# Kernel tuning notes

Measured on AMD Instinct MI355X. Metric: run time of the kernel, lower is better.

## Reference

```python
import jax, jax.numpy as jnp
import numpy as np

N = 50000
V_FEATS = 128
FILTERS = 128
K = 20


def setup_inputs() -> dict:
    key = jax.random.key(0)
    ks = jax.random.split(key, 8)
    vertices = jax.random.normal(ks[0], (N, V_FEATS), dtype=jnp.float32)
    nh_indices = jax.random.randint(ks[1], (N, K), 0, N, dtype=jnp.int32)
    int_idx = jax.random.randint(ks[2], (N, K), 0, N, dtype=jnp.int32)
    mask = jax.random.uniform(ks[3], (N, K)) < 0.3
    int_indices = jnp.where(mask, jnp.int32(-1), int_idx)
    nh_edges = jax.random.normal(ks[4], (N, K), dtype=jnp.float32)
    int_edges = jax.random.normal(ks[5], (N, K), dtype=jnp.float32)
    # kaiming-uniform-ish init for params
    bound = float(np.sqrt(6.0 / V_FEATS))
    Wvc = jax.random.uniform(ks[6], (V_FEATS, FILTERS), minval=-bound, maxval=bound, dtype=jnp.float32)
    Wvn = jax.random.uniform(ks[7], (V_FEATS, FILTERS), minval=-bound, maxval=bound, dtype=jnp.float32)
    bv = jnp.zeros((FILTERS,), dtype=jnp.float32)
    return {"vertices": vertices, "nh_indices": nh_indices, "int_indices": int_indices,
            "nh_edges": nh_edges, "int_edges": int_edges, "Wvc": Wvc, "Wvn": Wvn, "bv": bv}


def reference(vertices, nh_indices, int_indices, nh_edges, int_edges, Wvc, Wvn, bv):
    # [N, 2K] concatenated neighbor + interface indices / edge weights
    indices = jnp.concatenate([nh_indices, int_indices], axis=1)
    edges = jnp.concatenate([nh_edges, int_edges], axis=1)[..., None]  # [N,2K,1]
    part = (indices != -1).astype(vertices.dtype)[..., None]           # [N,2K,1] validity mask
    Zc = vertices @ Wvc                                                # [N,F] center term
    v_Wvn = vertices @ Wvn                                             # [N,F]
    gathered = v_Wvn[indices]  # [N,2K,F]; -1 wraps to last row, zeroed by mask (same as torch)
    denom = jnp.sum(indices > -1, axis=1, keepdims=True).astype(vertices.dtype)  # [N,1]
    Zn = jnp.sum(gathered * part * edges, axis=1) / denom             # [N,F]
    z = jax.nn.relu(Zc + Zn + bv)
    return z
```

## Files before the change

kernel.cpp:

```cpp
#include <hip/hip_runtime.h>

#define NV 50000
#define F 128
#define K 20
#define KCAT 256
#define RPB 32

typedef __attribute__((ext_vector_type(8))) __bf16 bf16x8;
typedef __attribute__((ext_vector_type(4))) float f32x4;
typedef __attribute__((ext_vector_type(2))) float f32x2;

__device__ inline ushort f2bf(float x) {
    uint u = __float_as_uint(x);
    return (ushort)((u + 0x7fffu + ((u >> 16) & 1u)) >> 16);
}


__global__ __launch_bounds__(256) void prep_kernel(
    const f32x4* __restrict__ v4, ushort* __restrict__ vb,
    uchar* __restrict__ v8,
    const float* __restrict__ Wvc, const float* __restrict__ Wvn,
    ushort* __restrict__ wt)
{
    int bid = blockIdx.x;
    if (bid < NV * F / 4 / 256) {
        int t = bid * 256 + threadIdx.x;
        int e = t * 4;
        int row = e >> 7, f = e & 127;
        f32x4 x = __builtin_nontemporal_load(v4 + t);
        uint2 o;
        o.x = (uint)f2bf(x[0]) | ((uint)f2bf(x[1]) << 16);
        o.y = (uint)f2bf(x[2]) | ((uint)f2bf(x[3]) << 16);
        *reinterpret_cast<uint2*>(vb + (size_t)row * KCAT + f) = o;
        int p8 = __builtin_amdgcn_cvt_pk_fp8_f32(x[0], x[1], 0, false);
        p8     = __builtin_amdgcn_cvt_pk_fp8_f32(x[2], x[3], p8, true);
        *reinterpret_cast<uint*>(v8 + (size_t)row * F + f) = (uint)p8;
    } else {
        int t = (bid - NV * F / 4 / 256) * 256 + threadIdx.x;
        int c = t >> 8, k = t & 255;
        float w = (k < F) ? Wvc[k * F + c] : Wvn[(k - F) * F + c];
        wt[t] = f2bf(w);
    }
}

__global__ __launch_bounds__(256) void agg_fp8(
    const uchar* __restrict__ v8,
    const int* __restrict__ nh_idx, const int* __restrict__ int_idx,
    const float* __restrict__ nh_e, const float* __restrict__ int_e,
    ushort* __restrict__ vb)
{
    __shared__ int2 sJW[RPB][2 * K + 1];
    __shared__ int  sCnt[RPB];

    const int tid = threadIdx.x;
    const int r0  = blockIdx.x * RPB;

    if (tid < RPB) sCnt[tid] = K;
    for (int x = tid; x < RPB * K; x += 256) {
        int r = x / K, k = x - r * K;
        int row = r0 + r;
        int2 jw = make_int2(0, 0);
        if (row < NV) {
            long g = (long)row * K + k;
            jw = make_int2(nh_idx[g], __float_as_int(nh_e[g]));
        }
        sJW[r][k] = jw;
    }
    __syncthreads();
    for (int x = tid; x < RPB * K; x += 256) {
        int r = x / K, k = x - r * K;
        int row = r0 + r;
        int2 jw = make_int2(0, 0);
        bool valid = false;
        if (row < NV) {
            long g = (long)row * K + k;
            int   j = int_idx[g];
            float w = int_e[g];
            valid = (j >= 0);
            jw = make_int2(valid ? j : 0, valid ? __float_as_int(w) : 0);
        }
        sJW[r][K + k] = jw;
        if (valid) atomicAdd(&sCnt[r], 1);
    }
    __syncthreads();

    const int lane  = tid & 63;
    const int wave  = tid >> 6;
    const int chunk = lane & 7;
    const int rw    = (wave << 3) + (lane >> 3);
    const uchar* __restrict__ src = v8 + chunk * 16;

    float acc[16];
    #pragma unroll
    for (int i = 0; i < 16; ++i) acc[i] = 0.f;

    #pragma unroll 4
    for (int k = 0; k < 2 * K; ++k) {
        int2  jw = sJW[rw][k];
        float w  = __int_as_float(jw.y);
        uint4 p  = *reinterpret_cast<const uint4*>(src + (size_t)jw.x * F);
        f32x2 f0 = __builtin_amdgcn_cvt_pk_f32_fp8(p.x, false);
        f32x2 f1 = __builtin_amdgcn_cvt_pk_f32_fp8(p.x, true);
        f32x2 f2 = __builtin_amdgcn_cvt_pk_f32_fp8(p.y, false);
        f32x2 f3 = __builtin_amdgcn_cvt_pk_f32_fp8(p.y, true);
        f32x2 f4 = __builtin_amdgcn_cvt_pk_f32_fp8(p.z, false);
        f32x2 f5 = __builtin_amdgcn_cvt_pk_f32_fp8(p.z, true);
        f32x2 f6 = __builtin_amdgcn_cvt_pk_f32_fp8(p.w, false);
        f32x2 f7 = __builtin_amdgcn_cvt_pk_f32_fp8(p.w, true);
        acc[0]  = fmaf(w, f0[0], acc[0]);   acc[1]  = fmaf(w, f0[1], acc[1]);
        acc[2]  = fmaf(w, f1[0], acc[2]);   acc[3]  = fmaf(w, f1[1], acc[3]);
        acc[4]  = fmaf(w, f2[0], acc[4]);   acc[5]  = fmaf(w, f2[1], acc[5]);
        acc[6]  = fmaf(w, f3[0], acc[6]);   acc[7]  = fmaf(w, f3[1], acc[7]);
        acc[8]  = fmaf(w, f4[0], acc[8]);   acc[9]  = fmaf(w, f4[1], acc[9]);
        acc[10] = fmaf(w, f5[0], acc[10]);  acc[11] = fmaf(w, f5[1], acc[11]);
        acc[12] = fmaf(w, f6[0], acc[12]);  acc[13] = fmaf(w, f6[1], acc[13]);
        acc[14] = fmaf(w, f7[0], acc[14]);  acc[15] = fmaf(w, f7[1], acc[15]);
    }

    const int row = r0 + rw;
    if (row < NV) {
        float inv = 1.f / (float)sCnt[rw];
        uint4 o0, o1;
        o0.x = (uint)f2bf(acc[0]  * inv) | ((uint)f2bf(acc[1]  * inv) << 16);
        o0.y = (uint)f2bf(acc[2]  * inv) | ((uint)f2bf(acc[3]  * inv) << 16);
        o0.z = (uint)f2bf(acc[4]  * inv) | ((uint)f2bf(acc[5]  * inv) << 16);
        o0.w = (uint)f2bf(acc[6]  * inv) | ((uint)f2bf(acc[7]  * inv) << 16);
        o1.x = (uint)f2bf(acc[8]  * inv) | ((uint)f2bf(acc[9]  * inv) << 16);
        o1.y = (uint)f2bf(acc[10] * inv) | ((uint)f2bf(acc[11] * inv) << 16);
        o1.z = (uint)f2bf(acc[12] * inv) | ((uint)f2bf(acc[13] * inv) << 16);
        o1.w = (uint)f2bf(acc[14] * inv) | ((uint)f2bf(acc[15] * inv) << 16);
        uint4* dst = reinterpret_cast<uint4*>(vb + (size_t)row * KCAT + F + chunk * 16);
        dst[0] = o0;
        dst[1] = o1;
    }
}

__global__ __launch_bounds__(256) void gemm_fused(
    const ushort* __restrict__ vb,
    const ushort* __restrict__ wt,
    const float* __restrict__ bv,
    float* __restrict__ out)
{
    const int lane = threadIdx.x & 63;
    const int wave = threadIdx.x >> 6;
    const int r0   = blockIdx.x * 64 + wave * 16;

    int arow = r0 + (lane & 15);
    if (arow >= NV) arow = NV - 1;

    const bf16x8* abase = reinterpret_cast<const bf16x8*>(
        vb + (size_t)arow * KCAT + (lane >> 4) * 8);
    bf16x8 a[8];
    #pragma unroll
    for (int ks = 0; ks < 8; ++ks)
        a[ks] = __builtin_nontemporal_load(abase + ks * 4);

    const ushort* wbase = wt + (size_t)(lane & 15) * KCAT + (lane >> 4) * 8;
    const int col0  = lane & 15;
    const int rbase = r0 + (lane >> 4) * 4;

    #pragma unroll 1
    for (int ct = 0; ct < 8; ++ct) {
        const bf16x8* wb = reinterpret_cast<const bf16x8*>(
            wbase + (size_t)ct * 16 * KCAT);
        f32x4 acc = (f32x4){0.f, 0.f, 0.f, 0.f};
        #pragma unroll
        for (int ks = 0; ks < 8; ++ks) {
            bf16x8 b = wb[ks * 4];
            acc = __builtin_amdgcn_mfma_f32_16x16x32_bf16(a[ks], b, acc, 0, 0, 0);
        }
        int c = ct * 16 + col0;
        float bb = bv[c];
        #pragma unroll
        for (int reg = 0; reg < 4; ++reg) {
            int r = rbase + reg;
            if (r < NV) {
                float z = acc[reg] + bb;
                __builtin_nontemporal_store(fmaxf(z, 0.f), out + (size_t)r * F + c);
            }
        }
    }
}

extern "C" void kernel_launch(void* const* d_in, const int* in_sizes, int n_in,
                              void* d_out, int out_size, void* d_ws, size_t ws_size,
                              hipStream_t stream)
{
    const float* v       = (const float*)d_in[0];
    const int*   nh_idx  = (const int*)  d_in[1];
    const int*   int_idx = (const int*)  d_in[2];
    const float* nh_e    = (const float*)d_in[3];
    const float* int_e   = (const float*)d_in[4];
    const float* Wvc     = (const float*)d_in[5];
    const float* Wvn     = (const float*)d_in[6];
    const float* bv      = (const float*)d_in[7];
    float* out = (float*)d_out;

    ushort* vb = (ushort*)d_ws;
    ushort* wt = vb + (size_t)NV * KCAT;
    uchar*  v8 = (uchar*)(wt + (size_t)F * KCAT);

    prep_kernel<<<NV * F / 4 / 256 + F * KCAT / 256, 256, 0, stream>>>(
        (const f32x4*)v, vb, v8, Wvc, Wvn, wt);
    agg_fp8<<<(NV + RPB - 1) / RPB, 256, 0, stream>>>(v8, nh_idx, int_idx,
                                                      nh_e, int_e, vb);
    gemm_fused<<<(NV + 63) / 64, 256, 0, stream>>>(vb, wt, bv, out);
}
```

Before: 156.2 us.

## Fuse neighbor aggregation and GEMM into one kernel via LDS staging

Merges the fp8 gather-aggregate kernel and the bf16 MFMA GEMM into one kernel. The aggregated rows are kept in shared memory instead of being written to and re-read from a global bf16 buffer. The center-term A operand is now read as fp32 and converted to bf16 inside the kernel, so the prep kernel no longer writes a bf16 copy of the vertices. Each block handles 64 rows in two aggregation passes, which saves a launch and global traffic at the cost of more LDS per block and possibly lower occupancy.

```diff
diff --git a/kernel.cpp b/kernel.cpp
--- a/kernel.cpp
+++ b/kernel.cpp
@@ -4,7 +4,8 @@
 #define F 128
 #define K 20
 #define KCAT 256
-#define RPB 32
+#define RPB 64
+#define LDSW (F + 8)
 
 typedef __attribute__((ext_vector_type(8))) __bf16 bf16x8;
 typedef __attribute__((ext_vector_type(4))) float f32x4;
@@ -17,8 +18,7 @@
 
 
 __global__ __launch_bounds__(256) void prep_kernel(
-    const f32x4* __restrict__ v4, ushort* __restrict__ vb,
-    uchar* __restrict__ v8,
+    const f32x4* __restrict__ v4, uchar* __restrict__ v8,
     const float* __restrict__ Wvc, const float* __restrict__ Wvn,
     ushort* __restrict__ wt)
 {
@@ -28,10 +28,6 @@
         int e = t * 4;
         int row = e >> 7, f = e & 127;
         f32x4 x = __builtin_nontemporal_load(v4 + t);
-        uint2 o;
-        o.x = (uint)f2bf(x[0]) | ((uint)f2bf(x[1]) << 16);
-        o.y = (uint)f2bf(x[2]) | ((uint)f2bf(x[3]) << 16);
-        *reinterpret_cast<uint2*>(vb + (size_t)row * KCAT + f) = o;
         int p8 = __builtin_amdgcn_cvt_pk_fp8_f32(x[0], x[1], 0, false);
         p8     = __builtin_amdgcn_cvt_pk_fp8_f32(x[2], x[3], p8, true);
         *reinterpret_cast<uint*>(v8 + (size_t)row * F + f) = (uint)p8;
@@ -43,14 +39,18 @@
     }
 }
 
-__global__ __launch_bounds__(256) void agg_fp8(
+__global__ __launch_bounds__(256) void fused_kernel(
+    const float* __restrict__ v,
     const uchar* __restrict__ v8,
     const int* __restrict__ nh_idx, const int* __restrict__ int_idx,
     const float* __restrict__ nh_e, const float* __restrict__ int_e,
-    ushort* __restrict__ vb)
+    const ushort* __restrict__ wt,
+    const float* __restrict__ bv,
+    float* __restrict__ out)
 {
-    __shared__ int2 sJW[RPB][2 * K + 1];
-    __shared__ int  sCnt[RPB];
+    __shared__ int2   sJW[RPB][2 * K + 1];
+    __shared__ int    sCnt[RPB];
+    __shared__ ushort sVA[RPB][LDSW];
 
     const int tid = threadIdx.x;
     const int r0  = blockIdx.x * RPB;
@@ -87,38 +87,37 @@
     const int lane  = tid & 63;
     const int wave  = tid >> 6;
     const int chunk = lane & 7;
-    const int rw    = (wave << 3) + (lane >> 3);
-    const uchar* __restrict__ src = v8 + chunk * 16;
-
-    float acc[16];
-    #pragma unroll
-    for (int i = 0; i < 16; ++i) acc[i] = 0.f;
-
-    #pragma unroll 4
-    for (int k = 0; k < 2 * K; ++k) {
-        int2  jw = sJW[rw][k];
-        float w  = __int_as_float(jw.y);
-        uint4 p  = *reinterpret_cast<const uint4*>(src + (size_t)jw.x * F);
-        f32x2 f0 = __builtin_amdgcn_cvt_pk_f32_fp8(p.x, false);
-        f32x2 f1 = __builtin_amdgcn_cvt_pk_f32_fp8(p.x, true);
-        f32x2 f2 = __builtin_amdgcn_cvt_pk_f32_fp8(p.y, false);
-        f32x2 f3 = __builtin_amdgcn_cvt_pk_f32_fp8(p.y, true);
-        f32x2 f4 = __builtin_amdgcn_cvt_pk_f32_fp8(p.z, false);
-        f32x2 f5 = __builtin_amdgcn_cvt_pk_f32_fp8(p.z, true);
-        f32x2 f6 = __builtin_amdgcn_cvt_pk_f32_fp8(p.w, false);
-        f32x2 f7 = __builtin_amdgcn_cvt_pk_f32_fp8(p.w, true);
-        acc[0]  = fmaf(w, f0[0], acc[0]);   acc[1]  = fmaf(w, f0[1], acc[1]);
-        acc[2]  = fmaf(w, f1[0], acc[2]);   acc[3]  = fmaf(w, f1[1], acc[3]);
-        acc[4]  = fmaf(w, f2[0], acc[4]);   acc[5]  = fmaf(w, f2[1], acc[5]);
-        acc[6]  = fmaf(w, f3[0], acc[6]);   acc[7]  = fmaf(w, f3[1], acc[7]);
-        acc[8]  = fmaf(w, f4[0], acc[8]);   acc[9]  = fmaf(w, f4[1], acc[9]);
-        acc[10] = fmaf(w, f5[0], acc[10]);  acc[11] = fmaf(w, f5[1], acc[11]);
-        acc[12] = fmaf(w, f6[0], acc[12]);  acc[13] = fmaf(w, f6[1], acc[13]);
-        acc[14] = fmaf(w, f7[0], acc[14]);  acc[15] = fmaf(w, f7[1], acc[15]);
-    }
-
-    const int row = r0 + rw;
-    if (row < NV) {
+    const uchar* __restrict__ gsrc = v8 + chunk * 16;
+
+    #pragma unroll 1
+    for (int pass = 0; pass < 2; ++pass) {
+        const int rw = pass * 32 + (wave << 3) + (lane >> 3);
+        float acc[16];
+        #pragma unroll
+        for (int i = 0; i < 16; ++i) acc[i] = 0.f;
+
+        #pragma unroll 4
+        for (int k = 0; k < 2 * K; ++k) {
+            int2  jw = sJW[rw][k];
+            float w  = __int_as_float(jw.y);
+            uint4 p  = *reinterpret_cast<const uint4*>(gsrc + (size_t)jw.x * F);
+            f32x2 f0 = __builtin_amdgcn_cvt_pk_f32_fp8(p.x, false);
+            f32x2 f1 = __builtin_amdgcn_cvt_pk_f32_fp8(p.x, true);
+            f32x2 f2 = __builtin_amdgcn_cvt_pk_f32_fp8(p.y, false);
+            f32x2 f3 = __builtin_amdgcn_cvt_pk_f32_fp8(p.y, true);
+            f32x2 f4 = __builtin_amdgcn_cvt_pk_f32_fp8(p.z, false);
+            f32x2 f5 = __builtin_amdgcn_cvt_pk_f32_fp8(p.z, true);
+            f32x2 f6 = __builtin_amdgcn_cvt_pk_f32_fp8(p.w, false);
+            f32x2 f7 = __builtin_amdgcn_cvt_pk_f32_fp8(p.w, true);
+            acc[0]  = fmaf(w, f0[0], acc[0]);   acc[1]  = fmaf(w, f0[1], acc[1]);
+            acc[2]  = fmaf(w, f1[0], acc[2]);   acc[3]  = fmaf(w, f1[1], acc[3]);
+            acc[4]  = fmaf(w, f2[0], acc[4]);   acc[5]  = fmaf(w, f2[1], acc[5]);
+            acc[6]  = fmaf(w, f3[0], acc[6]);   acc[7]  = fmaf(w, f3[1], acc[7]);
+            acc[8]  = fmaf(w, f4[0], acc[8]);   acc[9]  = fmaf(w, f4[1], acc[9]);
+            acc[10] = fmaf(w, f5[0], acc[10]);  acc[11] = fmaf(w, f5[1], acc[11]);
+            acc[12] = fmaf(w, f6[0], acc[12]);  acc[13] = fmaf(w, f6[1], acc[13]);
+            acc[14] = fmaf(w, f7[0], acc[14]);  acc[15] = fmaf(w, f7[1], acc[15]);
+        }
         float inv = 1.f / (float)sCnt[rw];
         uint4 o0, o1;
         o0.x = (uint)f2bf(acc[0]  * inv) | ((uint)f2bf(acc[1]  * inv) << 16);
@@ -129,35 +128,37 @@
         o1.y = (uint)f2bf(acc[10] * inv) | ((uint)f2bf(acc[11] * inv) << 16);
         o1.z = (uint)f2bf(acc[12] * inv) | ((uint)f2bf(acc[13] * inv) << 16);
         o1.w = (uint)f2bf(acc[14] * inv) | ((uint)f2bf(acc[15] * inv) << 16);
-        uint4* dst = reinterpret_cast<uint4*>(vb + (size_t)row * KCAT + F + chunk * 16);
+        uint4* dst = reinterpret_cast<uint4*>(&sVA[rw][chunk * 16]);
         dst[0] = o0;
         dst[1] = o1;
     }
-}
-
-__global__ __launch_bounds__(256) void gemm_fused(
-    const ushort* __restrict__ vb,
-    const ushort* __restrict__ wt,
-    const float* __restrict__ bv,
-    float* __restrict__ out)
-{
-    const int lane = threadIdx.x & 63;
-    const int wave = threadIdx.x >> 6;
-    const int r0   = blockIdx.x * 64 + wave * 16;
-
-    int arow = r0 + (lane & 15);
+    __syncthreads();
+
+    const int rloc = wave * 16 + (lane & 15);
+    int arow = r0 + rloc;
     if (arow >= NV) arow = NV - 1;
-
-    const bf16x8* abase = reinterpret_cast<const bf16x8*>(
-        vb + (size_t)arow * KCAT + (lane >> 4) * 8);
+    const int g = lane >> 4;
+
     bf16x8 a[8];
     #pragma unroll
-    for (int ks = 0; ks < 8; ++ks)
-        a[ks] = __builtin_nontemporal_load(abase + ks * 4);
-
-    const ushort* wbase = wt + (size_t)(lane & 15) * KCAT + (lane >> 4) * 8;
+    for (int kk = 0; kk < 4; ++kk) {
+        const float* vp = v + (size_t)arow * F + g * 8 + kk * 32;
+        f32x4 x0 = *reinterpret_cast<const f32x4*>(vp);
+        f32x4 x1 = *reinterpret_cast<const f32x4*>(vp + 4);
+        union { bf16x8 vv; ushort s[8]; } af;
+        af.s[0] = f2bf(x0[0]); af.s[1] = f2bf(x0[1]);
+        af.s[2] = f2bf(x0[2]); af.s[3] = f2bf(x0[3]);
+        af.s[4] = f2bf(x1[0]); af.s[5] = f2bf(x1[1]);
+        af.s[6] = f2bf(x1[2]); af.s[7] = f2bf(x1[3]);
+        a[kk] = af.vv;
+    }
+    #pragma unroll
+    for (int kk = 0; kk < 4; ++kk)
+        a[4 + kk] = *reinterpret_cast<const bf16x8*>(&sVA[rloc][g * 8 + kk * 32]);
+
+    const ushort* wbase = wt + (size_t)(lane & 15) * KCAT + g * 8;
     const int col0  = lane & 15;
-    const int rbase = r0 + (lane >> 4) * 4;
+    const int rbase = r0 + wave * 16 + g * 4;
 
     #pragma unroll 1
     for (int ct = 0; ct < 8; ++ct) {
@@ -196,13 +197,11 @@
     const float* bv      = (const float*)d_in[7];
     float* out = (float*)d_out;
 
-    ushort* vb = (ushort*)d_ws;
-    ushort* wt = vb + (size_t)NV * KCAT;
-    uchar*  v8 = (uchar*)(wt + (size_t)F * KCAT);
+    uchar*  v8 = (uchar*)d_ws;
+    ushort* wt = (ushort*)(v8 + (size_t)NV * F);
 
     prep_kernel<<<NV * F / 4 / 256 + F * KCAT / 256, 256, 0, stream>>>(
-        (const f32x4*)v, vb, v8, Wvc, Wvn, wt);
-    agg_fp8<<<(NV + RPB - 1) / RPB, 256, 0, stream>>>(v8, nh_idx, int_idx,
-                                                      nh_e, int_e, vb);
-    gemm_fused<<<(NV + 63) / 64, 256, 0, stream>>>(vb, wt, bv, out);
-}
+        (const f32x4*)v, v8, Wvc, Wvn, wt);
+    fused_kernel<<<(NV + RPB - 1) / RPB, 256, 0, stream>>>(
+        v, v8, nh_idx, int_idx, nh_e, int_e, wt, bv, out);
+}
```

Measured after the change: 152.1 us. 2.6% less time.
